# Kernel tuning notes

Measured on AMD Instinct MI355X. Metric: run time of the kernel, lower is better.

Reference implementation:

```python
import jax, jax.numpy as jnp
import numpy as np

NQ = 4
NL = 3
HEADS = 8

_H = jnp.asarray(np.array([[1, 1], [1, -1]], np.complex64) / np.sqrt(2.0))
_X = jnp.asarray(np.array([[0, 1], [1, 0]], np.complex64))
_Y = jnp.asarray(np.array([[0, -1j], [1j, 0]], np.complex64))
_Z = jnp.asarray(np.array([[1, 0], [0, -1]], np.complex64))
_CNOT = jnp.asarray(np.array([[1, 0, 0, 0], [0, 1, 0, 0], [0, 0, 0, 1], [0, 0, 1, 0]], np.complex64))


def _rx(t):
    c = jnp.cos(t / 2).astype(jnp.complex64)
    s = (-1j * jnp.sin(t / 2)).astype(jnp.complex64)
    return jnp.stack([jnp.stack([c, s]), jnp.stack([s, c])])


def _ry(t):
    c = jnp.cos(t / 2).astype(jnp.complex64)
    s = jnp.sin(t / 2).astype(jnp.complex64)
    return jnp.stack([jnp.stack([c, -s]), jnp.stack([s, c])])


def _rz(t):
    e = jnp.exp((-0.5j) * t).astype(jnp.complex64)
    z = jnp.zeros((), jnp.complex64)
    return jnp.stack([jnp.stack([e, z]), jnp.stack([z, jnp.conj(e)])])


def _crx(t):
    # control-RX in |control,target> basis
    return jnp.eye(4, dtype=jnp.complex64).at[2:, 2:].set(_rx(t))


def _ap1(psi, U, q):
    # apply 2x2 gate U on qubit axis q of psi:(2,2,2,2)
    return jnp.moveaxis(jnp.tensordot(U, psi, axes=[[1], [q]]), 0, q)


def _ap2(psi, U, q1, q2):
    p = jnp.moveaxis(psi, (q1, q2), (0, 1)).reshape(4, 4)
    p = (U @ p).reshape(2, 2, 2, 2)
    return jnp.moveaxis(p, (0, 1), (q1, q2))


def _expv(psi, P, q):
    return jnp.real(jnp.vdot(psi, _ap1(psi, P, q)))


def _circuit(inp, w, ew, gam, bet):
    # inp:(4,)  w,ew:(3,4)  gam,bet:(3,)  -> (12,) expvals Z,X,Y
    psi = jnp.zeros((16,), jnp.complex64).at[0].set(1.0).reshape(2, 2, 2, 2)
    for i in range(NQ):  # AngleEmbedding(rotation='Y')
        psi = _ap1(psi, _ry(inp[i]), i)
    for L in range(NL):
        for i in range(NQ):
            psi = _ap1(psi, _rx(w[L, i]), i)
            psi = _ap1(psi, _ry(w[L, i]), i)
            psi = _ap1(psi, _rz(w[L, i]), i)
        for i in range(NQ):  # CRX entangling ring
            psi = _ap2(psi, _crx(ew[L, i]), i, (i + 1) % NQ)
        # Grover diffusion
        for q in range(NQ):
            psi = _ap1(psi, _H, q)
        for q in range(NQ):
            psi = _ap1(psi, _X, q)
        psi = _ap1(psi, _H, NQ - 1)
        psi = psi.at[1, 1, 1, :].set(psi[1, 1, 1, ::-1])  # CCCX ctrl=[0,1,2] tgt=3
        psi = _ap1(psi, _H, NQ - 1)
        for q in range(NQ):
            psi = _ap1(psi, _X, q)
        for q in range(NQ):
            psi = _ap1(psi, _H, q)
        # QAOA cost + mixer
        for i in range(NQ - 1):
            psi = _ap2(psi, _CNOT, i, i + 1)
            psi = _ap1(psi, _rz(gam[L]), i + 1)
            psi = _ap2(psi, _CNOT, i, i + 1)
        for q in range(NQ):
            psi = _ap1(psi, _rx(bet[L]), q)
    meas = [_expv(psi, _Z, q) for q in range(NQ)]
    meas += [_expv(psi, _X, q) for q in range(NQ)]
    meas += [_expv(psi, _Y, q) for q in range(NQ)]
    return jnp.stack(meas)


_vqc = jax.vmap(_circuit, in_axes=(0, None, None, None, None))


def _layernorm(x, g, b, eps=1e-5):
    mu = jnp.mean(x, -1, keepdims=True)
    var = jnp.mean((x - mu) ** 2, -1, keepdims=True)
    return (x - mu) * jax.lax.rsqrt(var + eps) * g + b


def _qtransform(xf, Wp, bp, ln_g, ln_b, w, ew, gam, bet):
    p = jnp.tanh(xf @ Wp.T + bp)  # (BS,4)
    p = _layernorm(p, ln_g, ln_b)
    return _vqc(p, w, ew, gam, bet)  # (BS,12)


def setup_inputs() -> dict:
    key = jax.random.key(0)
    ks = jax.random.split(key, 32)
    B, S, Hd = 4, 1024, 512
    d = {"x": jax.random.normal(ks[0], (B, S, Hd), jnp.float32)}
    d["Wp"] = jax.random.normal(ks[1], (NQ, Hd), jnp.float32) * 0.05
    d["bp"] = jnp.zeros((NQ,), jnp.float32)
    d["ln_g"] = jnp.ones((NQ,), jnp.float32)
    d["ln_b"] = jnp.zeros((NQ,), jnp.float32)
    i = 2
    for pfx in ["q", "k", "v"]:
        d[pfx + "w"] = 0.01 * jax.random.normal(ks[i], (NL, NQ), jnp.float32)
        d[pfx + "e"] = 0.01 * jax.random.normal(ks[i + 1], (NL, NQ), jnp.float32)
        d[pfx + "g"] = 0.01 * jax.random.normal(ks[i + 2], (NL,), jnp.float32)
        d[pfx + "b"] = 0.01 * jax.random.normal(ks[i + 3], (NL,), jnp.float32)
        i += 4
    fused = 3 * NQ
    d["Wq"] = jax.random.normal(ks[i], (Hd, fused), jnp.float32) * 0.2
    d["bq"] = jnp.zeros((Hd,), jnp.float32)
    d["Wk"] = jax.random.normal(ks[i + 1], (Hd, fused), jnp.float32) * 0.2
    d["bk"] = jnp.zeros((Hd,), jnp.float32)
    d["Wv"] = jax.random.normal(ks[i + 2], (Hd, fused), jnp.float32) * 0.2
    d["bv"] = jnp.zeros((Hd,), jnp.float32)
    d["Wo"] = jax.random.normal(ks[i + 3], (Hd, Hd), jnp.float32) * 0.05
    d["bo"] = jnp.zeros((Hd,), jnp.float32)
    return d


def reference(x, Wp, bp, ln_g, ln_b, qw, qe, qg, qb, kw, ke, kg, kb, vw, ve, vg, vb,
              Wq, bq, Wk, bk, Wv, bv, Wo, bo):
    B, S, Hd = x.shape
    hd = Hd // HEADS
    xf = x.reshape(B * S, Hd)
    tq = _qtransform(xf, Wp, bp, ln_g, ln_b, qw, qe, qg, qb)
    tk = _qtransform(xf, Wp, bp, ln_g, ln_b, kw, ke, kg, kb)
    tv = _qtransform(xf, Wp, bp, ln_g, ln_b, vw, ve, vg, vb)
    q = (tq @ Wq.T + bq).reshape(B, S, HEADS, hd)
    k = (tk @ Wk.T + bk).reshape(B, S, HEADS, hd)
    v = (tv @ Wv.T + bv).reshape(B, S, HEADS, hd)
    scale = float(hd) ** 0.5
    attn = jax.nn.softmax(jnp.einsum('bqhd,bkhd->bhqk', q, k) / scale, axis=-1)
    out = jnp.einsum('bhqk,bkhd->bqhd', attn, v).reshape(B, S, Hd)
    return out @ Wo.T + bo
```

## Files before the change

kernel.cpp:

```cpp
#include <hip/hip_runtime.h>
#include <hip/hip_bf16.h>
#include <math.h>

#define NROWS 4096
#define HD 512
#define HEADS 8
#define HDD 64
#define SEQ 1024
#define QSCALE 0.18033688011112042f

typedef unsigned short u16;
typedef __attribute__((ext_vector_type(8))) short sh8;
typedef __attribute__((ext_vector_type(4))) float f4;

__device__ __forceinline__ f4 mfma16(sh8 a, sh8 b, f4 c) {
  return __builtin_amdgcn_mfma_f32_16x16x32_bf16(a, b, c, 0, 0, 0);
}

__device__ __forceinline__ u16 f2bf(float x) {
  union { float f; unsigned u; } v; v.f = x;
  unsigned r = v.u + 0x7fff + ((v.u >> 16) & 1);
  return (u16)(r >> 16);
}

#define SWZA(r, cb) ((((r) * 128) + (cb)) ^ (((r) & 7) << 4))
#define SWZB(r, cb) ((((r) * 256) + (cb)) ^ (((r) & 7) << 4))

__global__ __launch_bounds__(256) void k_prep(
    const float* __restrict__ qw, const float* __restrict__ qe,
    const float* __restrict__ qg, const float* __restrict__ qb,
    const float* __restrict__ kw, const float* __restrict__ ke,
    const float* __restrict__ kg, const float* __restrict__ kb,
    const float* __restrict__ vw, const float* __restrict__ ve,
    const float* __restrict__ vg, const float* __restrict__ vb,
    float* __restrict__ Mout) {
  const int c = blockIdx.x;
  const int tid = threadIdx.x;
  __shared__ float aC[32], aS[32];
  __shared__ float GT[60][8];
  __shared__ int   GM[60][2];
  __shared__ float PF[3][16][2];
  __shared__ float SR[16][17], SI[16][17];
  __shared__ float TS[16], TI[16];
  __shared__ float Ur[256], Ui[256];

  const float* w = (c == 0) ? qw : (c == 1) ? kw : vw;
  const float* e = (c == 0) ? qe : (c == 1) ? ke : ve;
  const float* g = (c == 0) ? qg : (c == 1) ? kg : vg;
  const float* b = (c == 0) ? qb : (c == 1) ? kb : vb;

  if (tid < 30) {
    float ang = (tid < 12) ? w[tid] : (tid < 24) ? e[tid - 12]
               : (tid < 27) ? g[tid - 24] : b[tid - 27];
    float s_, c_;
    sincosf(0.5f * ang, &s_, &c_);
    aC[tid] = c_; aS[tid] = s_;
  }
  __syncthreads();

  if (tid < 60) {
    int L = tid / 20, s5 = tid % 20;
    int typ, aidx, M, C;
    if (s5 < 12) {
      int q = s5 / 3; typ = s5 % 3; aidx = L * 4 + q; M = 8 >> q; C = 0;
    } else if (s5 < 16) {
      int q = s5 - 12; typ = 0; aidx = 12 + L * 4 + q;
      C = 8 >> q; M = 8 >> ((q + 1) & 3);
    } else {
      int q = s5 - 16; typ = 0; aidx = 27 + L; M = 8 >> q; C = 0;
    }
    float cc = aC[aidx], ss = aS[aidx];
    float u0r = cc, u0i = 0.f, u1r = 0.f, u1i = 0.f,
          u2r = 0.f, u2i = 0.f, u3r = cc, u3i = 0.f;
    if (typ == 0)      { u1i = -ss; u2i = -ss; }
    else if (typ == 1) { u1r = -ss; u2r = ss; }
    else               { u0i = -ss; u3i = ss; }
    GT[tid][0] = u0r; GT[tid][1] = u0i; GT[tid][2] = u1r; GT[tid][3] = u1i;
    GT[tid][4] = u2r; GT[tid][5] = u2i; GT[tid][6] = u3r; GT[tid][7] = u3i;
    GM[tid][0] = M; GM[tid][1] = C;
  }
  if (tid >= 64 && tid < 112) {
    int idx = tid - 64, L = idx >> 4, a = idx & 15;
    float cg = aC[24 + L], sg = aS[24 + L];
    float c2 = cg * cg - sg * sg, s2 = 2.f * cg * sg;
    float c3 = cg * c2 - sg * s2, s3 = cg * s2 + sg * c2;
    int u = (a ^ (a >> 1)) & 7;
    int n = (u & 1) + ((u >> 1) & 1) + ((u >> 2) & 1);
    PF[L][a][0] = (n == 0 || n == 3) ? c3 : cg;
    PF[L][a][1] = (n == 0) ? -s3 : (n == 1) ? -sg : (n == 2) ? sg : s3;
  }
  for (int i = tid; i < 256; i += 256) {
    SR[i >> 4][i & 15] = (i >> 4) == (i & 15) ? 1.f : 0.f;
    SI[i >> 4][i & 15] = 0.f;
  }
  __syncthreads();

  const int p = tid >> 4, col = tid & 15;
  for (int L = 0; L < 3; ++L) {
    for (int s5 = 0; s5 < 16; ++s5) {
      if (tid < 128) {
        int gi = L * 20 + s5;
        const float* u = GT[gi];
        int M = GM[gi][0], C = GM[gi][1];
        int lo = p & (M - 1);
        int a = ((p - lo) << 1) | lo;
        int bb = a | M;
        bool act = (C == 0) | ((a & C) != 0);
        float ar = SR[a][col], ai = SI[a][col];
        float br = SR[bb][col], bi = SI[bb][col];
        float nar = u[0]*ar - u[1]*ai + u[2]*br - u[3]*bi;
        float nai = u[0]*ai + u[1]*ar + u[2]*bi + u[3]*br;
        float nbr = u[4]*ar - u[5]*ai + u[6]*br - u[7]*bi;
        float nbi = u[4]*ai + u[5]*ar + u[6]*bi + u[7]*br;
        SR[a][col]  = act ? nar : ar;  SI[a][col]  = act ? nai : ai;
        SR[bb][col] = act ? nbr : br;  SI[bb][col] = act ? nbi : bi;
      }
      __syncthreads();
    }
    if (tid < 16) {
      float sR = 0.f, sI = 0.f;
      for (int a = 0; a < 16; ++a) { sR += SR[a][tid]; sI += SI[a][tid]; }
      TS[tid] = sR * 0.125f; TI[tid] = sI * 0.125f;
    }
    __syncthreads();
    if (tid < 128) {
      for (int k = 0; k < 2; ++k) {
        int a = 2 * p + k;
        float vr = SR[a][col] - TS[col];
        float vi = SI[a][col] - TI[col];
        float pc = PF[L][a][0], ps = PF[L][a][1];
        SR[a][col] = vr * pc - vi * ps;
        SI[a][col] = vr * ps + vi * pc;
      }
    }
    __syncthreads();
    for (int s5 = 16; s5 < 20; ++s5) {
      if (tid < 128) {
        int gi = L * 20 + s5;
        const float* u = GT[gi];
        int M = GM[gi][0];
        int lo = p & (M - 1);
        int a = ((p - lo) << 1) | lo;
        int bb = a | M;
        float ar = SR[a][col], ai = SI[a][col];
        float br = SR[bb][col], bi = SI[bb][col];
        SR[a][col]  = u[0]*ar - u[1]*ai + u[2]*br - u[3]*bi;
        SI[a][col]  = u[0]*ai + u[1]*ar + u[2]*bi + u[3]*br;
        SR[bb][col] = u[4]*ar - u[5]*ai + u[6]*br - u[7]*bi;
        SI[bb][col] = u[4]*ai + u[5]*ar + u[6]*bi + u[7]*br;
      }
      __syncthreads();
    }
  }

  for (int i = tid; i < 256; i += 256) {
    Ur[i] = SR[i >> 4][i & 15];
    Ui[i] = SI[i >> 4][i & 15];
  }
  __syncthreads();

  if (tid < 192) {
    const int j = tid >> 4, a = tid & 15;
    const int typ = j >> 2;
    const int Mm = 8 >> (j & 3);
    float ax[4] = {0.f,0.f,0.f,0.f}, ay[4] = {0.f,0.f,0.f,0.f},
          az[4] = {0.f,0.f,0.f,0.f}, aw[4] = {0.f,0.f,0.f,0.f};
#pragma clang loop unroll_count(4)
    for (int k = 0; k < 16; ++k) {
      float uar = Ur[k * 16 + a], uai = Ui[k * 16 + a];
      int k2; float cR, cI;
      if (typ == 0)      { k2 = k;      float z = (k & Mm) ? -1.f : 1.f; cR = z*uar; cI = z*uai; }
      else if (typ == 1) { k2 = k ^ Mm; cR = uar; cI = uai; }
      else               { k2 = k ^ Mm; float sg = (k & Mm) ? 1.f : -1.f; cR = sg*uai; cI = -sg*uar; }
      const float* ur2 = Ur + k2 * 16;
      const float* ui2 = Ui + k2 * 16;
#pragma unroll
      for (int i = 0; i < 4; ++i) {
        ax[i] += cR * ur2[i*4+0] + cI * ui2[i*4+0];
        ay[i] += cR * ur2[i*4+1] + cI * ui2[i*4+1];
        az[i] += cR * ur2[i*4+2] + cI * ui2[i*4+2];
        aw[i] += cR * ur2[i*4+3] + cI * ui2[i*4+3];
      }
    }
    float* dst = Mout + ((c * 12 + j) * 16 + a) * 16;
#pragma unroll
    for (int i = 0; i < 4; ++i)
      ((float4*)dst)[i] = make_float4(ax[i], ay[i], az[i], aw[i]);
  }
}

__global__ __launch_bounds__(256) void k_fused(const float* __restrict__ x,
    const float* __restrict__ Wp, const float* __restrict__ bp,
    const float* __restrict__ ln_g, const float* __restrict__ ln_b,
    const float* __restrict__ Mg,
    const float* __restrict__ Wq, const float* __restrict__ bq,
    const float* __restrict__ Wk, const float* __restrict__ bk,
    const float* __restrict__ Wv, const float* __restrict__ bv,
    u16* __restrict__ Qo, u16* __restrict__ Ko, u16* __restrict__ Vto) {
  const int rb = blockIdx.x;
  const int tid = threadIdx.x;
  __shared__ float Ml[3][12][256];
  __shared__ float pl[16][4];
  __shared__ float psil[16][17];
  __shared__ float tt[3][16][12];

  {
    const float4* src = (const float4*)Mg;
    float4* dst = (float4*)&Ml[0][0][0];
    for (int i = tid; i < 2304; i += 256) dst[i] = src[i];
  }

  const int w = tid >> 6, lane = tid & 63;
  {
    float4 wpa[4], wpb[4];
#pragma unroll
    for (int j = 0; j < 4; ++j) {
      wpa[j] = *(const float4*)(Wp + j * HD + lane * 8);
      wpb[j] = *(const float4*)(Wp + j * HD + lane * 8 + 4);
    }
    for (int i = 0; i < 4; ++i) {
      int r = w * 4 + i;
      const float* xr = x + (rb * 16 + r) * HD + lane * 8;
      float4 xa = *(const float4*)xr, xb = *(const float4*)(xr + 4);
      float acc[4];
#pragma unroll
      for (int j = 0; j < 4; ++j)
        acc[j] = xa.x*wpa[j].x + xa.y*wpa[j].y + xa.z*wpa[j].z + xa.w*wpa[j].w
               + xb.x*wpb[j].x + xb.y*wpb[j].y + xb.z*wpb[j].z + xb.w*wpb[j].w;
#pragma unroll
      for (int j = 0; j < 4; ++j)
#pragma unroll
        for (int off = 32; off >= 1; off >>= 1)
          acc[j] += __shfl_xor(acc[j], off);
      if (lane == 0) {
        float v0 = tanhf(acc[0] + bp[0]);
        float v1 = tanhf(acc[1] + bp[1]);
        float v2 = tanhf(acc[2] + bp[2]);
        float v3 = tanhf(acc[3] + bp[3]);
        float mu = 0.25f * (v0 + v1 + v2 + v3);
        float d0 = v0 - mu, d1 = v1 - mu, d2 = v2 - mu, d3 = v3 - mu;
        float inv = rsqrtf(0.25f * (d0*d0 + d1*d1 + d2*d2 + d3*d3) + 1e-5f);
        pl[r][0] = d0 * inv * ln_g[0] + ln_b[0];
        pl[r][1] = d1 * inv * ln_g[1] + ln_b[1];
        pl[r][2] = d2 * inv * ln_g[2] + ln_b[2];
        pl[r][3] = d3 * inv * ln_g[3] + ln_b[3];
      }
    }
  }
  __syncthreads();

  if (tid < 16) {
    float cs[4], sn[4];
    sincosf(0.5f * pl[tid][0], &sn[0], &cs[0]);
    sincosf(0.5f * pl[tid][1], &sn[1], &cs[1]);
    sincosf(0.5f * pl[tid][2], &sn[2], &cs[2]);
    sincosf(0.5f * pl[tid][3], &sn[3], &cs[3]);
    float q01[4] = {cs[0]*cs[1], cs[0]*sn[1], sn[0]*cs[1], sn[0]*sn[1]};
    float q23[4] = {cs[2]*cs[3], cs[2]*sn[3], sn[2]*cs[3], sn[2]*sn[3]};
#pragma unroll
    for (int a = 0; a < 16; ++a) psil[tid][a] = q01[a >> 2] * q23[a & 3];
  }
  __syncthreads();

  if (tid < 192) {
    const int r = tid & 15, j = tid >> 4;
    float psi[16];
#pragma unroll
    for (int a = 0; a < 16; ++a) psi[a] = psil[r][a];
#pragma clang loop unroll(disable)
    for (int c = 0; c < 3; ++c) {
      const float* Mj = &Ml[c][j][0];
      float y = 0.f;
#pragma unroll
      for (int a = 0; a < 16; ++a) {
        float rsum = 0.f;
#pragma unroll
        for (int i = 0; i < 16; ++i) rsum += Mj[a*16+i] * psi[i];
        y += psi[a] * rsum;
      }
      tt[c][r][j] = y;
    }
  }
  __syncthreads();

  const int n0 = rb * 16, b = n0 >> 10, ss0 = n0 & 1023;
  {
    const int o0 = tid * 2;
    float wq0[12], wq1[12], wk0[12], wk1[12];
#pragma unroll
    for (int j = 0; j < 12; ++j) {
      wq0[j] = Wq[o0*12 + j];  wq1[j] = Wq[(o0+1)*12 + j];
      wk0[j] = Wk[o0*12 + j];  wk1[j] = Wk[(o0+1)*12 + j];
    }
    const float bq0 = bq[o0], bq1 = bq[o0+1], bk0 = bk[o0], bk1 = bk[o0+1];
    const int h = o0 >> 6, d = o0 & 63;
    u16* qrow = Qo + ((b * HEADS + h) * SEQ + ss0) * HDD + d;
    u16* krow = Ko + ((b * HEADS + h) * SEQ + ss0) * HDD + d;
    for (int rr = 0; rr < 16; ++rr) {
      float a0 = bq0, a1 = bq1, c0 = bk0, c1 = bk1;
#pragma unroll
      for (int j = 0; j < 12; ++j) {
        float tq = tt[0][rr][j], tk = tt[1][rr][j];
        a0 += tq * wq0[j]; a1 += tq * wq1[j];
        c0 += tk * wk0[j]; c1 += tk * wk1[j];
      }
      unsigned qv = (unsigned)f2bf(a0 * QSCALE) | ((unsigned)f2bf(a1 * QSCALE) << 16);
      unsigned kv = (unsigned)f2bf(c0) | ((unsigned)f2bf(c1) << 16);
      *(unsigned*)(qrow + rr * HDD) = qv;
      *(unsigned*)(krow + rr * HDD) = kv;
    }
  }
  {
    const int sp = tid & 7, gg = tid >> 3;
    const int r0 = 2 * sp, r1 = r0 + 1;
    for (int i = 0; i < 16; ++i) {
      int o = gg + 32 * i;
      float v0 = bv[o], v1 = bv[o];
#pragma unroll
      for (int j = 0; j < 12; ++j) {
        float wv = Wv[o * 12 + j];
        v0 += tt[2][r0][j] * wv;
        v1 += tt[2][r1][j] * wv;
      }
      unsigned vv = (unsigned)f2bf(v0) | ((unsigned)f2bf(v1) << 16);
      *(unsigned*)(Vto + (b * 512 + o) * SEQ + ss0 + r0) = vv;
    }
  }
}

__global__ __launch_bounds__(256) void k_attn_mfma(const u16* __restrict__ Q,
    const u16* __restrict__ K, const u16* __restrict__ Vt,
    u16* __restrict__ Ob) {
  const int bh = blockIdx.y, qt = blockIdx.x;
  const int tid = threadIdx.x, w = tid >> 6, l = tid & 63;
  const int lr = l & 15, lh = l >> 4;

  __shared__ u16 Kl[2][128 * 64];
  __shared__ u16 Vl[2][64 * 128];
  __shared__ u16 Pl[4][16 * 128];

  const u16* Qb = Q + (bh * SEQ + qt * 64) * HDD;
  const u16* Kb = K + bh * SEQ * HDD;
  const u16* Vb = Vt + bh * HDD * SEQ;

  sh8 qf[2];
#pragma unroll
  for (int kk = 0; kk < 2; ++kk)
    qf[kk] = *(const sh8*)(Qb + (w * 16 + lr) * HDD + kk * 32 + lh * 8);

  f4 oacc[4];
  float lsum[4] = {0.f, 0.f, 0.f, 0.f};
#pragma unroll
  for (int n = 0; n < 4; ++n) oacc[n] = (f4){0.f, 0.f, 0.f, 0.f};

  sh8 kreg[4], vreg[4];

#define STAGE_LOAD(ch) { \
    _Pragma("unroll") \
    for (int i = 0; i < 4; ++i) { \
      int idx = i * 256 + tid; \
      kreg[i] = *(const sh8*)(Kb + ((ch) * 128 + (idx >> 3)) * HDD + (idx & 7) * 8); \
      vreg[i] = *(const sh8*)(Vb + (idx >> 4) * SEQ + (ch) * 128 + (idx & 15) * 8); \
    } }
#define STAGE_WRITE(buf) { \
    _Pragma("unroll") \
    for (int i = 0; i < 4; ++i) { \
      int idx = i * 256 + tid; \
      *(sh8*)((char*)Kl[buf] + SWZA(idx >> 3, (idx & 7) * 16)) = kreg[i]; \
      *(sh8*)((char*)Vl[buf] + SWZB(idx >> 4, (idx & 15) * 16)) = vreg[i]; \
    } }

  STAGE_LOAD(0)
  STAGE_WRITE(0)
  __syncthreads();

  for (int ch = 0; ch < SEQ / 128; ++ch) {
    const int cur = ch & 1;
    if (ch < 7) STAGE_LOAD(ch + 1)

    f4 sacc[8];
#pragma unroll
    for (int n = 0; n < 8; ++n) sacc[n] = (f4){0.f, 0.f, 0.f, 0.f};
#pragma unroll
    for (int kk = 0; kk < 2; ++kk) {
#pragma unroll
      for (int n = 0; n < 8; ++n) {
        sh8 kf = *(const sh8*)((const char*)Kl[cur] + SWZA(n * 16 + lr, kk * 64 + lh * 16));
        sacc[n] = mfma16(qf[kk], kf, sacc[n]);
      }
    }

#pragma unroll
    for (int n = 0; n < 8; ++n) {
#pragma unroll
      for (int r = 0; r < 4; ++r) {
        float pv = exp2f(sacc[n][r]);
        lsum[r] += pv;
        *(u16*)((char*)Pl[w] + SWZB(lh * 4 + r, (n * 16 + lr) * 2)) = f2bf(pv);
      }
    }

#pragma unroll
    for (int kk = 0; kk < 4; ++kk) {
      sh8 pf = *(const sh8*)((const char*)Pl[w] + SWZB(lr, kk * 64 + lh * 16));
#pragma unroll
      for (int n = 0; n < 4; ++n) {
        sh8 vf = *(const sh8*)((const char*)Vl[cur] + SWZB(n * 16 + lr, kk * 64 + lh * 16));
        oacc[n] = mfma16(pf, vf, oacc[n]);
      }
    }

    if (ch < 7) STAGE_WRITE(cur ^ 1)
    __syncthreads();
  }
#undef STAGE_LOAD
#undef STAGE_WRITE

#pragma unroll
  for (int r = 0; r < 4; ++r) {
    lsum[r] += __shfl_xor(lsum[r], 1); lsum[r] += __shfl_xor(lsum[r], 2);
    lsum[r] += __shfl_xor(lsum[r], 4); lsum[r] += __shfl_xor(lsum[r], 8);
  }

  int bb = bh >> 3, h = bh & 7;
#pragma unroll
  for (int r = 0; r < 4; ++r) {
    int row = qt * 64 + w * 16 + lh * 4 + r;
    float inv = 1.f / lsum[r];
#pragma unroll
    for (int n = 0; n < 4; ++n)
      Ob[(bb * SEQ + row) * HD + h * 64 + n * 16 + lr] = f2bf(oacc[n][r] * inv);
  }
}

__global__ __launch_bounds__(256) void k_oproj_mfma(const u16* __restrict__ A,
    const float* __restrict__ W, const float* __restrict__ bo,
    float* __restrict__ out) {
  const int nb = blockIdx.x, ob = blockIdx.y;
  const int tid = threadIdx.x, w = tid >> 6, l = tid & 63;
  const int lr = l & 15, lh = l >> 4;
  __shared__ u16 Al[64 * 64];
  __shared__ u16 Wl[64 * 64];
  f4 acc[4];
#pragma unroll
  for (int n = 0; n < 4; ++n) acc[n] = (f4){0.f, 0.f, 0.f, 0.f};
  for (int ch = 0; ch < 8; ++ch) {
    __syncthreads();
#pragma unroll
    for (int i = 0; i < 2; ++i) {
      int idx = i * 256 + tid;
      int r = idx >> 3, c8 = idx & 7;
      *(sh8*)((char*)Al + SWZA(r, c8 * 16)) =
          *(const sh8*)(A + (nb * 64 + r) * HD + ch * 64 + c8 * 8);
      const float* wp = W + (ob * 64 + r) * HD + ch * 64 + c8 * 8;
      float4 f0 = *(const float4*)wp;
      float4 f1 = *(const float4*)(wp + 4);
      sh8 wv;
      wv[0] = (short)f2bf(f0.x); wv[1] = (short)f2bf(f0.y);
      wv[2] = (short)f2bf(f0.z); wv[3] = (short)f2bf(f0.w);
      wv[4] = (short)f2bf(f1.x); wv[5] = (short)f2bf(f1.y);
      wv[6] = (short)f2bf(f1.z); wv[7] = (short)f2bf(f1.w);
      *(sh8*)((char*)Wl + SWZA(r, c8 * 16)) = wv;
    }
    __syncthreads();
#pragma unroll
    for (int kk = 0; kk < 2; ++kk) {
      sh8 af = *(const sh8*)((const char*)Al + SWZA(w * 16 + lr, kk * 64 + lh * 16));
#pragma unroll
      for (int n = 0; n < 4; ++n) {
        sh8 wf = *(const sh8*)((const char*)Wl + SWZA(n * 16 + lr, kk * 64 + lh * 16));
        acc[n] = mfma16(af, wf, acc[n]);
      }
    }
  }
#pragma unroll
  for (int r = 0; r < 4; ++r) {
    int row = nb * 64 + w * 16 + lh * 4 + r;
#pragma unroll
    for (int n = 0; n < 4; ++n) {
      int col = ob * 64 + n * 16 + lr;
      out[row * HD + col] = acc[n][r] + bo[col];
    }
  }
}

extern "C" void kernel_launch(void* const* d_in, const int* in_sizes, int n_in,
                              void* d_out, int out_size, void* d_ws, size_t ws_size,
                              hipStream_t stream) {
  const float* x    = (const float*)d_in[0];
  const float* Wp   = (const float*)d_in[1];
  const float* bp   = (const float*)d_in[2];
  const float* ln_g = (const float*)d_in[3];
  const float* ln_b = (const float*)d_in[4];
  const float* qw   = (const float*)d_in[5];
  const float* qe   = (const float*)d_in[6];
  const float* qg   = (const float*)d_in[7];
  const float* qb_  = (const float*)d_in[8];
  const float* kw   = (const float*)d_in[9];
  const float* ke   = (const float*)d_in[10];
  const float* kg   = (const float*)d_in[11];
  const float* kb_  = (const float*)d_in[12];
  const float* vw   = (const float*)d_in[13];
  const float* ve   = (const float*)d_in[14];
  const float* vg   = (const float*)d_in[15];
  const float* vb_  = (const float*)d_in[16];
  const float* Wq   = (const float*)d_in[17];
  const float* bq   = (const float*)d_in[18];
  const float* Wk   = (const float*)d_in[19];
  const float* bk   = (const float*)d_in[20];
  const float* Wv   = (const float*)d_in[21];
  const float* bv   = (const float*)d_in[22];
  const float* Wo   = (const float*)d_in[23];
  const float* bo   = (const float*)d_in[24];

  float* ws   = (float*)d_ws;
  float* Mbuf = ws;
  u16* qb  = (u16*)(Mbuf + 9216);
  u16* kb  = qb + 32 * SEQ * HDD;
  u16* vtb = kb + 32 * SEQ * HDD;
  u16* ab  = vtb + 32 * SEQ * HDD;

  k_prep<<<3, 256, 0, stream>>>(qw, qe, qg, qb_, kw, ke, kg, kb_,
                                vw, ve, vg, vb_, Mbuf);
  k_fused<<<NROWS / 16, 256, 0, stream>>>(x, Wp, bp, ln_g, ln_b, Mbuf,
                                          Wq, bq, Wk, bk, Wv, bv, qb, kb, vtb);
  dim3 ga(SEQ / 64, 32);
  k_attn_mfma<<<ga, 256, 0, stream>>>(qb, kb, vtb, ab);
  dim3 go(NROWS / 64, HD / 64);
  k_oproj_mfma<<<go, 256, 0, stream>>>(ab, Wo, bo, (float*)d_out);
}
```

Measured before the change: 86.42 us.

## Compute QKV projection with MFMA using bf16-packed weights prepared in k_prep

k_prep gains three blocks that convert Wq/Wk/Wv and their biases into padded bf16 rows, with the Q scale and the bias folded in as an extra K column. k_fused writes the quantum features as bf16 into a K=32 padded tile with a constant 1 column, then runs the 12→512 projections with 16x16x32 bf16 MFMA instead of scalar FP32 loops. The M matrix copy in LDS is also XOR-swizzled and read as float4 to cut bank conflicts. The projection inputs and weights now carry bf16 rounding, which adds precision loss, and the Q/K stores become scattered 2-byte writes.

```diff
diff --git a/kernel.cpp b/kernel.cpp
--- a/kernel.cpp
+++ b/kernel.cpp
@@ -10,6 +10,7 @@
 #define QSCALE 0.18033688011112042f
 
 typedef unsigned short u16;
+typedef unsigned int u32;
 typedef __attribute__((ext_vector_type(8))) short sh8;
 typedef __attribute__((ext_vector_type(4))) float f4;
 
@@ -33,9 +34,34 @@
     const float* __restrict__ kg, const float* __restrict__ kb,
     const float* __restrict__ vw, const float* __restrict__ ve,
     const float* __restrict__ vg, const float* __restrict__ vb,
-    float* __restrict__ Mout) {
+    const float* __restrict__ Wq, const float* __restrict__ bq,
+    const float* __restrict__ Wk, const float* __restrict__ bk,
+    const float* __restrict__ Wv, const float* __restrict__ bv,
+    float* __restrict__ Mout, u16* __restrict__ Wbout) {
   const int c = blockIdx.x;
   const int tid = threadIdx.x;
+
+  if (c >= 3) {
+    const int c2 = c - 3;
+    const float* W = (c2 == 0) ? Wq : (c2 == 1) ? Wk : Wv;
+    const float* bb = (c2 == 0) ? bq : (c2 == 1) ? bk : bv;
+    const float sc = (c2 == 0) ? QSCALE : 1.f;
+    for (int o = tid; o < 512; o += 256) {
+      unsigned out[16];
+#pragma unroll
+      for (int i = 0; i < 16; ++i) out[i] = 0u;
+      const float* wr = W + o * 12;
+#pragma unroll
+      for (int jp = 0; jp < 6; ++jp)
+        out[jp] = (unsigned)f2bf(wr[2*jp] * sc) | ((unsigned)f2bf(wr[2*jp+1] * sc) << 16);
+      out[6] = (unsigned)f2bf(bb[o] * sc);
+      unsigned* dst = (unsigned*)(Wbout + (c2 * 512 + o) * 32);
+#pragma unroll
+      for (int i = 0; i < 16; ++i) dst[i] = out[i];
+    }
+    return;
+  }
+
   __shared__ float aC[32], aS[32];
   __shared__ float GT[60][8];
   __shared__ int   GM[60][2];
@@ -192,22 +218,24 @@
 __global__ __launch_bounds__(256) void k_fused(const float* __restrict__ x,
     const float* __restrict__ Wp, const float* __restrict__ bp,
     const float* __restrict__ ln_g, const float* __restrict__ ln_b,
-    const float* __restrict__ Mg,
-    const float* __restrict__ Wq, const float* __restrict__ bq,
-    const float* __restrict__ Wk, const float* __restrict__ bk,
-    const float* __restrict__ Wv, const float* __restrict__ bv,
+    const float* __restrict__ Mg, const u16* __restrict__ Wb,
     u16* __restrict__ Qo, u16* __restrict__ Ko, u16* __restrict__ Vto) {
   const int rb = blockIdx.x;
   const int tid = threadIdx.x;
-  __shared__ float Ml[3][12][256];
+  __shared__ float Ml[3 * 12 * 256];
   __shared__ float pl[16][4];
   __shared__ float psil[16][17];
-  __shared__ float tt[3][16][12];
+  __shared__ u16 tb[3 * 16 * 32];
 
   {
     const float4* src = (const float4*)Mg;
-    float4* dst = (float4*)&Ml[0][0][0];
-    for (int i = tid; i < 2304; i += 256) dst[i] = src[i];
+    for (int f = tid; f < 2304; f += 256) {
+      int cj = f >> 6, e4 = f & 63;
+      int j = cj % 12;
+      ((float4*)Ml)[cj * 64 + (e4 ^ (j & 7))] = src[f];
+    }
+    for (int i = tid; i < 768; i += 256) ((u32*)tb)[i] = 0u;
+    if (tid < 48) tb[(tid >> 4) * 512 + (tid & 15) * 32 + 12] = 0x3F80;
   }
 
   const int w = tid >> 6, lane = tid & 63;
@@ -269,61 +297,48 @@
     for (int a = 0; a < 16; ++a) psi[a] = psil[r][a];
 #pragma clang loop unroll(disable)
     for (int c = 0; c < 3; ++c) {
-      const float* Mj = &Ml[c][j][0];
+      const float4* Mj = (const float4*)(Ml + (c * 12 + j) * 256);
       float y = 0.f;
 #pragma unroll
       for (int a = 0; a < 16; ++a) {
         float rsum = 0.f;
 #pragma unroll
-        for (int i = 0; i < 16; ++i) rsum += Mj[a*16+i] * psi[i];
+        for (int i = 0; i < 4; ++i) {
+          float4 m4 = Mj[(a * 4 + i) ^ (j & 7)];
+          rsum += m4.x*psi[i*4] + m4.y*psi[i*4+1] + m4.z*psi[i*4+2] + m4.w*psi[i*4+3];
+        }
         y += psi[a] * rsum;
       }
-      tt[c][r][j] = y;
-    }
-  }
-  __syncthreads();
-
-  const int n0 = rb * 16, b = n0 >> 10, ss0 = n0 & 1023;
-  {
-    const int o0 = tid * 2;
-    float wq0[12], wq1[12], wk0[12], wk1[12];
-#pragma unroll
-    for (int j = 0; j < 12; ++j) {
-      wq0[j] = Wq[o0*12 + j];  wq1[j] = Wq[(o0+1)*12 + j];
-      wk0[j] = Wk[o0*12 + j];  wk1[j] = Wk[(o0+1)*12 + j];
-    }
-    const float bq0 = bq[o0], bq1 = bq[o0+1], bk0 = bk[o0], bk1 = bk[o0+1];
-    const int h = o0 >> 6, d = o0 & 63;
-    u16* qrow = Qo + ((b * HEADS + h) * SEQ + ss0) * HDD + d;
-    u16* krow = Ko + ((b * HEADS + h) * SEQ + ss0) * HDD + d;
-    for (int rr = 0; rr < 16; ++rr) {
-      float a0 = bq0, a1 = bq1, c0 = bk0, c1 = bk1;
-#pragma unroll
-      for (int j = 0; j < 12; ++j) {
-        float tq = tt[0][rr][j], tk = tt[1][rr][j];
-        a0 += tq * wq0[j]; a1 += tq * wq1[j];
-        c0 += tk * wk0[j]; c1 += tk * wk1[j];
-      }
-      unsigned qv = (unsigned)f2bf(a0 * QSCALE) | ((unsigned)f2bf(a1 * QSCALE) << 16);
-      unsigned kv = (unsigned)f2bf(c0) | ((unsigned)f2bf(c1) << 16);
-      *(unsigned*)(qrow + rr * HDD) = qv;
-      *(unsigned*)(krow + rr * HDD) = kv;
-    }
-  }
-  {
-    const int sp = tid & 7, gg = tid >> 3;
-    const int r0 = 2 * sp, r1 = r0 + 1;
-    for (int i = 0; i < 16; ++i) {
-      int o = gg + 32 * i;
-      float v0 = bv[o], v1 = bv[o];
-#pragma unroll
-      for (int j = 0; j < 12; ++j) {
-        float wv = Wv[o * 12 + j];
-        v0 += tt[2][r0][j] * wv;
-        v1 += tt[2][r1][j] * wv;
-      }
-      unsigned vv = (unsigned)f2bf(v0) | ((unsigned)f2bf(v1) << 16);
-      *(unsigned*)(Vto + (b * 512 + o) * SEQ + ss0 + r0) = vv;
+      tb[c * 512 + r * 32 + j] = f2bf(y);
+    }
+  }
+  __syncthreads();
+
+  const int lr = lane & 15, lh = lane >> 4;
+  const int b = rb >> 6, ss0 = (rb & 63) * 16;
+  const f4 zero4 = (f4){0.f, 0.f, 0.f, 0.f};
+#pragma unroll
+  for (int c = 0; c < 3; ++c) {
+    sh8 af = *(const sh8*)(tb + c * 512 + lr * 32 + lh * 8);
+#pragma unroll
+    for (int n = 0; n < 8; ++n) {
+      int o = (w * 8 + n) * 16 + lr;
+      sh8 bfr = *(const sh8*)(Wb + (c * 512 + o) * 32 + lh * 8);
+      f4 acc = mfma16(af, bfr, zero4);
+      if (c == 0) {
+        int base = ((b * HEADS + (o >> 6)) * SEQ + ss0 + lh * 4) * HDD + (o & 63);
+#pragma unroll
+        for (int r = 0; r < 4; ++r) Qo[base + r * HDD] = f2bf(acc[r]);
+      } else if (c == 1) {
+        int base = ((b * HEADS + (o >> 6)) * SEQ + ss0 + lh * 4) * HDD + (o & 63);
+#pragma unroll
+        for (int r = 0; r < 4; ++r) Ko[base + r * HDD] = f2bf(acc[r]);
+      } else {
+        unsigned long long vv =
+            (unsigned long long)((u32)f2bf(acc[0]) | ((u32)f2bf(acc[1]) << 16)) |
+            ((unsigned long long)((u32)f2bf(acc[2]) | ((u32)f2bf(acc[3]) << 16)) << 32);
+        *(unsigned long long*)(Vto + (b * 512 + o) * SEQ + ss0 + lh * 4) = vv;
+      }
     }
   }
 }
@@ -515,15 +530,17 @@
 
   float* ws   = (float*)d_ws;
   float* Mbuf = ws;
-  u16* qb  = (u16*)(Mbuf + 9216);
+  u16* Wbb = (u16*)(Mbuf + 9216);
+  u16* qb  = Wbb + 49152;
   u16* kb  = qb + 32 * SEQ * HDD;
   u16* vtb = kb + 32 * SEQ * HDD;
   u16* ab  = vtb + 32 * SEQ * HDD;
 
-  k_prep<<<3, 256, 0, stream>>>(qw, qe, qg, qb_, kw, ke, kg, kb_,
-                                vw, ve, vg, vb_, Mbuf);
-  k_fused<<<NROWS / 16, 256, 0, stream>>>(x, Wp, bp, ln_g, ln_b, Mbuf,
-                                          Wq, bq, Wk, bk, Wv, bv, qb, kb, vtb);
+  k_prep<<<6, 256, 0, stream>>>(qw, qe, qg, qb_, kw, ke, kg, kb_,
+                                vw, ve, vg, vb_, Wq, bq, Wk, bk, Wv, bv,
+                                Mbuf, Wbb);
+  k_fused<<<NROWS / 16, 256, 0, stream>>>(x, Wp, bp, ln_g, ln_b, Mbuf, Wbb,
+                                          qb, kb, vtb);
   dim3 ga(SEQ / 64, 32);
   k_attn_mfma<<<ga, 256, 0, stream>>>(qb, kb, vtb, ab);
   dim3 go(NROWS / 64, HD / 64);
```

New measurement: 84.80 us. Within noise of the previous version (-1.9%).
